# Optimization experiments

Measured on AMD Instinct MI355X. Metric: run time of the kernel, lower is better.

The kernel has to match this reference:

```python
import jax, jax.numpy as jnp
import numpy as np

D = 768  # in_channels == out_channels (forced by residual + shared LayerNorm)
B, S = 8, 2048


def setup_inputs() -> dict:
    key = jax.random.key(0)
    ks = jax.random.split(key, 5)
    x = jax.random.normal(ks[0], (B, S, D), dtype=jnp.float32)
    # LayerNorm params
    ln_g = jnp.ones((D,), dtype=jnp.float32)
    ln_b = jnp.zeros((D,), dtype=jnp.float32)
    # Q/K linear params (torch Linear: y = x @ W.T + b)
    scale = 1.0 / np.sqrt(D)
    Wq = jax.random.uniform(ks[1], (D, D), jnp.float32, -scale, scale)
    bq = jax.random.uniform(ks[2], (D,), jnp.float32, -scale, scale)
    Wk = jax.random.uniform(ks[3], (D, D), jnp.float32, -scale, scale)
    bk = jax.random.uniform(ks[4], (D,), jnp.float32, -scale, scale)
    return {"x": x, "ln_g": ln_g, "ln_b": ln_b, "Wq": Wq, "bq": bq, "Wk": Wk, "bk": bk}


def _layernorm(x, g, b, eps=1e-5):
    mu = jnp.mean(x, axis=-1, keepdims=True)
    var = jnp.mean(jnp.square(x - mu), axis=-1, keepdims=True)
    return (x - mu) * jax.lax.rsqrt(var + eps) * g + b


def reference(x, ln_g, ln_b, Wq, bq, Wk, bk):
    origin = x
    xn = _layernorm(x, ln_g, ln_b)
    Q = xn @ Wq.T + bq  # [B,S,D]
    K = xn @ Wk.T + bk  # [B,S,D]
    scores = jnp.einsum('bsd,btd->bst', Q, K) / jnp.sqrt(jnp.asarray(D, x.dtype))
    attn = jax.nn.softmax(scores, axis=-1)  # [B,S,S]
    out = jnp.einsum('bst,btd->bsd', attn, origin) + origin
    # note: original then computes relu(layernorm(out)) but returns `out` (dead code)
    return out
```

## Files before the change

### kernel.cpp

```cpp
#include <hip/hip_runtime.h>

typedef __bf16 bf16;
typedef __bf16 v8bf __attribute__((ext_vector_type(8)));
typedef __bf16 v4bf __attribute__((ext_vector_type(4)));
typedef float  v4f  __attribute__((ext_vector_type(4)));

__device__ __forceinline__ void gload_lds16(const void* g, void* l) {
    __builtin_amdgcn_global_load_lds(
        (const __attribute__((address_space(1))) void*)g,
        (__attribute__((address_space(3))) void*)l, 16, 0, 0);
}

__global__ __launch_bounds__(256)
void ln_cast(const float* __restrict__ x, const float* __restrict__ g,
             const float* __restrict__ b, bf16* __restrict__ xn,
             bf16* __restrict__ xv)
{
    const long row = blockIdx.x;
    const float* xr = x + row * 768;
    const int tid = threadIdx.x;
    const int wave = tid >> 6, lane = tid & 63;

    float a0 = xr[tid], a1 = xr[tid + 256], a2 = xr[tid + 512];
    float s = a0 + a1 + a2;
    #pragma unroll
    for (int off = 32; off; off >>= 1) s += __shfl_xor(s, off);
    __shared__ float sh[4], sh2[4];
    if (!lane) sh[wave] = s;
    __syncthreads();
    const float mu = (sh[0] + sh[1] + sh[2] + sh[3]) * (1.0f / 768.0f);

    float d0 = a0 - mu, d1 = a1 - mu, d2 = a2 - mu;
    float ss = d0 * d0 + d1 * d1 + d2 * d2;
    #pragma unroll
    for (int off = 32; off; off >>= 1) ss += __shfl_xor(ss, off);
    if (!lane) sh2[wave] = ss;
    __syncthreads();
    const float var = (sh2[0] + sh2[1] + sh2[2] + sh2[3]) * (1.0f / 768.0f);
    const float rstd = rsqrtf(var + 1e-5f);

    bf16* xnr = xn + row * 768;
    bf16* xvr = xv + row * 768;
    xnr[tid]       = (bf16)(d0 * rstd * g[tid]       + b[tid]);
    xnr[tid + 256] = (bf16)(d1 * rstd * g[tid + 256] + b[tid + 256]);
    xnr[tid + 512] = (bf16)(d2 * rstd * g[tid + 512] + b[tid + 512]);
    xvr[tid]       = (bf16)a0;
    xvr[tid + 256] = (bf16)a1;
    xvr[tid + 512] = (bf16)a2;
}

__global__ __launch_bounds__(256)
void cvt_w(const float* __restrict__ Wq, const float* __restrict__ Wk,
           bf16* __restrict__ Wcat)
{
    const int z = blockIdx.y;
    const float* src = z ? Wk : Wq;
    bf16* dst = Wcat + (long)z * 768 * 768;
    const int i = (blockIdx.x * 256 + threadIdx.x) * 4;
    const float4 v = *(const float4*)(src + i);
    v4bf o = {(bf16)v.x, (bf16)v.y, (bf16)v.z, (bf16)v.w};
    *(v4bf*)(dst + i) = o;
}

__global__ __launch_bounds__(256)
void transpose_bf(const bf16* __restrict__ in, bf16* __restrict__ outT)
{
    __shared__ __attribute__((aligned(16))) bf16 tile[64 * 64];
    const int t0 = blockIdx.x * 64, d0 = blockIdx.y * 64;
    in   += (long)blockIdx.z * 2048 * 768;
    outT += (long)blockIdx.z * 768 * 2048;
    const int tid = threadIdx.x;

    #pragma unroll
    for (int it = 0; it < 2; ++it) {
        const int lin = it * 256 + tid;
        const int r = lin >> 3;
        const int g = lin & 7;
        const int pg = g ^ (r & 7) ^ ((r >> 3) & 7);
        v8bf v = *(const v8bf*)(in + (long)(t0 + r) * 768 + d0 + g * 8);
        *(v8bf*)(tile + r * 64 + pg * 8) = v;
    }
    __syncthreads();
    #pragma unroll
    for (int it = 0; it < 2; ++it) {
        const int lin = it * 256 + tid;
        const int dd = lin >> 3;
        const int tb = lin & 7;
        v8bf o;
        #pragma unroll
        for (int j = 0; j < 8; ++j) {
            const int t = tb * 8 + j;
            const int pg = (dd >> 3) ^ (t & 7) ^ ((t >> 3) & 7);
            o[j] = tile[t * 64 + pg * 8 + (dd & 7)];
        }
        *(v8bf*)(outT + (long)(d0 + dd) * 2048 + t0 + tb * 8) = o;
    }
}

__global__ __launch_bounds__(256)
void gemm_qk(const bf16* __restrict__ A, const bf16* __restrict__ W,
             const float* __restrict__ bq, const float* __restrict__ bk,
             float qscale, bf16* __restrict__ Qb, bf16* __restrict__ Kb)
{
    __shared__ __attribute__((aligned(16))) bf16 As[2][128 * 32];
    __shared__ __attribute__((aligned(16))) bf16 Bs[2][128 * 32];

    const int bx = blockIdx.x;
    const int r = bx & 7, j = bx >> 3;
    const int m0 = (r * 16 + j / 12) * 128;
    const int n0 = (j % 12) * 128;

    const int tid = threadIdx.x, wave = tid >> 6, lane = tid & 63;
    const bf16* Ab = A + (long)m0 * 768;
    const bf16* Bb = W + (long)n0 * 768;

    const int lrow = lane >> 2;
    const int lk   = (lane & 3) * 8;
    const int wm = (wave >> 1) * 64, wn = (wave & 1) * 64;
    const int lr = lane & 15, lq = lane >> 4;

    v4f acc[4][4] = {};

    for (int kk = 0; kk < 768; kk += 64) {
        #pragma unroll
        for (int p = 0; p < 2; ++p)
            #pragma unroll
            for (int it = 0; it < 2; ++it) {
                const int c = it * 4 + wave;
                const int row = c * 16 + lrow;
                gload_lds16(Ab + (long)row * 768 + kk + p * 32 + lk,
                            (char*)As[p] + c * 1024);
                gload_lds16(Bb + (long)row * 768 + kk + p * 32 + lk,
                            (char*)Bs[p] + c * 1024);
            }
        __syncthreads();

        #pragma unroll
        for (int p = 0; p < 2; ++p) {
            v8bf af[4], bfr[4];
            #pragma unroll
            for (int i = 0; i < 4; ++i)
                af[i] = *(const v8bf*)(As[p] + (wm + i * 16 + lr) * 32 + lq * 8);
            #pragma unroll
            for (int jj = 0; jj < 4; ++jj)
                bfr[jj] = *(const v8bf*)(Bs[p] + (wn + jj * 16 + lr) * 32 + lq * 8);
            #pragma unroll
            for (int i = 0; i < 4; ++i)
                #pragma unroll
                for (int jj = 0; jj < 4; ++jj)
                    acc[i][jj] = __builtin_amdgcn_mfma_f32_16x16x32_bf16(
                        af[i], bfr[jj], acc[i][jj], 0, 0, 0);
        }
        __syncthreads();
    }

    const bool isQ = (n0 < 768);
    const float* bias = isQ ? bq : bk;
    const float sc = isQ ? qscale : 1.0f;
    bf16* C = isQ ? Qb : Kb;
    const int c0 = isQ ? n0 : n0 - 768;

    #pragma unroll
    for (int i = 0; i < 4; ++i) {
        #pragma unroll
        for (int rr = 0; rr < 4; ++rr) {
            const int row = m0 + wm + i * 16 + lq * 4 + rr;
            #pragma unroll
            for (int jj = 0; jj < 4; ++jj) {
                const int col = c0 + wn + jj * 16 + lr;
                C[(long)row * 768 + col] = (bf16)((acc[i][jj][rr] + bias[col]) * sc);
            }
        }
    }
}

__global__ __launch_bounds__(256)
void gemm_scores(const bf16* __restrict__ Q, const bf16* __restrict__ K,
                 bf16* __restrict__ S)
{
    __shared__ __attribute__((aligned(16))) bf16 As[2][128 * 32];
    __shared__ __attribute__((aligned(16))) bf16 Bs[2][128 * 32];

    const int bx = blockIdx.x;
    const int batch = bx & 7, j = bx >> 3;
    const int m0 = (j >> 4) * 128, n0 = (j & 15) * 128;

    const bf16* Ab = Q + (long)batch * 2048 * 768 + (long)m0 * 768;
    const bf16* Bb = K + (long)batch * 2048 * 768 + (long)n0 * 768;
    bf16* C = S + (long)batch * 2048 * 2048;

    const int tid = threadIdx.x, wave = tid >> 6, lane = tid & 63;
    const int lrow = lane >> 2;
    const int lk   = (lane & 3) * 8;
    const int wm = (wave >> 1) * 64, wn = (wave & 1) * 64;
    const int lr = lane & 15, lq = lane >> 4;

    v4f acc[4][4] = {};

    for (int kk = 0; kk < 768; kk += 64) {
        #pragma unroll
        for (int p = 0; p < 2; ++p)
            #pragma unroll
            for (int it = 0; it < 2; ++it) {
                const int c = it * 4 + wave;
                const int row = c * 16 + lrow;
                gload_lds16(Ab + (long)row * 768 + kk + p * 32 + lk,
                            (char*)As[p] + c * 1024);
                gload_lds16(Bb + (long)row * 768 + kk + p * 32 + lk,
                            (char*)Bs[p] + c * 1024);
            }
        __syncthreads();

        #pragma unroll
        for (int p = 0; p < 2; ++p) {
            v8bf af[4], bfr[4];
            #pragma unroll
            for (int i = 0; i < 4; ++i)
                af[i] = *(const v8bf*)(As[p] + (wm + i * 16 + lr) * 32 + lq * 8);
            #pragma unroll
            for (int jj = 0; jj < 4; ++jj)
                bfr[jj] = *(const v8bf*)(Bs[p] + (wn + jj * 16 + lr) * 32 + lq * 8);
            #pragma unroll
            for (int i = 0; i < 4; ++i)
                #pragma unroll
                for (int jj = 0; jj < 4; ++jj)
                    acc[i][jj] = __builtin_amdgcn_mfma_f32_16x16x32_bf16(
                        af[i], bfr[jj], acc[i][jj], 0, 0, 0);
        }
        __syncthreads();
    }

    #pragma unroll
    for (int i = 0; i < 4; ++i) {
        #pragma unroll
        for (int rr = 0; rr < 4; ++rr) {
            const int row = m0 + wm + i * 16 + lq * 4 + rr;
            #pragma unroll
            for (int jj = 0; jj < 4; ++jj) {
                const int col = n0 + wn + jj * 16 + lr;
                C[(long)row * 2048 + col] = (bf16)acc[i][jj][rr];
            }
        }
    }
}

__global__ __launch_bounds__(256)
void softmax_rows(bf16* __restrict__ S)
{
    const long row = blockIdx.x;
    bf16* p = S + row * 2048 + threadIdx.x * 8;
    const int wave = threadIdx.x >> 6, lane = threadIdx.x & 63;

    v8bf raw = *(const v8bf*)p;
    float v[8];
    float mx = -1e30f;
    #pragma unroll
    for (int j = 0; j < 8; ++j) { v[j] = (float)raw[j]; mx = fmaxf(mx, v[j]); }
    #pragma unroll
    for (int off = 32; off; off >>= 1) mx = fmaxf(mx, __shfl_xor(mx, off));
    __shared__ float shm[4], shs[4];
    if (!lane) shm[wave] = mx;
    __syncthreads();
    mx = fmaxf(fmaxf(shm[0], shm[1]), fmaxf(shm[2], shm[3]));

    float s = 0.f;
    #pragma unroll
    for (int j = 0; j < 8; ++j) { v[j] = __expf(v[j] - mx); s += v[j]; }
    #pragma unroll
    for (int off = 32; off; off >>= 1) s += __shfl_xor(s, off);
    if (!lane) shs[wave] = s;
    __syncthreads();
    const float inv = 1.0f / (shs[0] + shs[1] + shs[2] + shs[3]);

    v8bf o;
    #pragma unroll
    for (int j = 0; j < 8; ++j) o[j] = (bf16)(v[j] * inv);
    *(v8bf*)p = o;
}

__global__ __launch_bounds__(256)
void gemm_pv(const bf16* __restrict__ P, const bf16* __restrict__ VT,
             const float* __restrict__ Xres, float* __restrict__ Out)
{
    __shared__ __attribute__((aligned(16))) bf16 As[2][64 * 32];
    __shared__ __attribute__((aligned(16))) bf16 Bs[2][128 * 32];

    const int bx = blockIdx.x;
    const int batch = bx & 7, j = bx >> 3;
    const int m0 = (j / 6) * 64;
    const int n0 = (j % 6) * 128;

    const bf16* Ab = P  + (long)batch * 2048 * 2048 + (long)m0 * 2048;
    const bf16* Bb = VT + (long)batch * 768 * 2048  + (long)n0 * 2048;
    const float* Xr = Xres + (long)batch * 2048 * 768;
    float* O = Out + (long)batch * 2048 * 768;

    const int tid = threadIdx.x, wave = tid >> 6, lane = tid & 63;
    const int lrow = lane >> 2;
    const int lk   = (lane & 3) * 8;
    const int wm = (wave >> 1) * 32, wn = (wave & 1) * 64;
    const int lr = lane & 15, lq = lane >> 4;

    v4f acc[2][4] = {};

    for (int kk = 0; kk < 2048; kk += 64) {
        #pragma unroll
        for (int p = 0; p < 2; ++p) {
            gload_lds16(Ab + (long)(wave * 16 + lrow) * 2048 + kk + p * 32 + lk,
                        (char*)As[p] + wave * 1024);
            #pragma unroll
            for (int it = 0; it < 2; ++it) {
                const int c = it * 4 + wave;
                gload_lds16(Bb + (long)(c * 16 + lrow) * 2048 + kk + p * 32 + lk,
                            (char*)Bs[p] + c * 1024);
            }
        }
        __syncthreads();

        #pragma unroll
        for (int p = 0; p < 2; ++p) {
            v8bf af[2], bfr[4];
            #pragma unroll
            for (int i = 0; i < 2; ++i)
                af[i] = *(const v8bf*)(As[p] + (wm + i * 16 + lr) * 32 + lq * 8);
            #pragma unroll
            for (int jj = 0; jj < 4; ++jj)
                bfr[jj] = *(const v8bf*)(Bs[p] + (wn + jj * 16 + lr) * 32 + lq * 8);
            #pragma unroll
            for (int i = 0; i < 2; ++i)
                #pragma unroll
                for (int jj = 0; jj < 4; ++jj)
                    acc[i][jj] = __builtin_amdgcn_mfma_f32_16x16x32_bf16(
                        af[i], bfr[jj], acc[i][jj], 0, 0, 0);
        }
        __syncthreads();
    }

    #pragma unroll
    for (int i = 0; i < 2; ++i) {
        #pragma unroll
        for (int rr = 0; rr < 4; ++rr) {
            const int row = m0 + wm + i * 16 + lq * 4 + rr;
            #pragma unroll
            for (int jj = 0; jj < 4; ++jj) {
                const int col = n0 + wn + jj * 16 + lr;
                const long idx = (long)row * 768 + col;
                O[idx] = acc[i][jj][rr] + Xr[idx];
            }
        }
    }
}

extern "C" void kernel_launch(void* const* d_in, const int* in_sizes, int n_in,
                              void* d_out, int out_size, void* d_ws, size_t ws_size,
                              hipStream_t stream)
{
    const float* x    = (const float*)d_in[0];
    const float* ln_g = (const float*)d_in[1];
    const float* ln_b = (const float*)d_in[2];
    const float* Wq   = (const float*)d_in[3];
    const float* bq   = (const float*)d_in[4];
    const float* Wk   = (const float*)d_in[5];
    const float* bk   = (const float*)d_in[6];
    float* out = (float*)d_out;

    const long R = 8L * 2048;
    char* ws = (char*)d_ws;
    size_t off = 0;
    auto take = [&](size_t bytes) -> char* {
        char* p = ws + off;
        off += (bytes + 255) & ~(size_t)255;
        return p;
    };
    bf16* xn   = (bf16*)take(R * 768 * 2);
    bf16* xv   = (bf16*)take(R * 768 * 2);
    bf16* Qb   = (bf16*)take(R * 768 * 2);
    bf16* Kb   = (bf16*)take(R * 768 * 2);
    bf16* Wcat = (bf16*)take(1536L * 768 * 2);
    bf16* Sc   = (bf16*)take(8L * 2048 * 2048 * 2);

    ln_cast<<<R, 256, 0, stream>>>(x, ln_g, ln_b, xn, xv);
    cvt_w<<<dim3(576, 2), 256, 0, stream>>>(Wq, Wk, Wcat);

    const float qscale = 0.036084391824351615f;
    gemm_qk<<<1536, 256, 0, stream>>>(xn, Wcat, bq, bk, qscale, Qb, Kb);

    bf16* xvT = xn;
    transpose_bf<<<dim3(32, 12, 8), 256, 0, stream>>>(xv, xvT);

    gemm_scores<<<2048, 256, 0, stream>>>(Qb, Kb, Sc);
    softmax_rows<<<16384, 256, 0, stream>>>(Sc);
    gemm_pv<<<1536, 256, 0, stream>>>(Sc, xvT, x, out);
}
```

Before: 340.9 us.

## Fuse softmax exp into scores GEMM and defer normalization to PV epilogue

Removes the standalone softmax kernel. The scores GEMM epilogue now writes exp(score) directly and accumulates per-row sums with atomics into a buffer that ln_cast zeroes, and the PV GEMM divides by that row sum in its epilogue. The score tiles are also remapped into 4x4 groups to improve L2 reuse of Q and K. This saves a full read and write of the 8x2048x2048 bf16 score matrix and one launch. In exchange it drops max-subtraction, so exp can overflow if scores grow large, and the atomic row sums make the accumulation order nondeterministic.

```diff
diff --git a/kernel.cpp b/kernel.cpp
--- a/kernel.cpp
+++ b/kernel.cpp
@@ -14,12 +14,14 @@
 __global__ __launch_bounds__(256)
 void ln_cast(const float* __restrict__ x, const float* __restrict__ g,
              const float* __restrict__ b, bf16* __restrict__ xn,
-             bf16* __restrict__ xv)
+             bf16* __restrict__ xv, float* __restrict__ L)
 {
     const long row = blockIdx.x;
     const float* xr = x + row * 768;
     const int tid = threadIdx.x;
     const int wave = tid >> 6, lane = tid & 63;
+
+    if (row < 64) L[row * 256 + tid] = 0.0f;
 
     float a0 = xr[tid], a1 = xr[tid + 256], a2 = xr[tid + 512];
     float s = a0 + a1 + a2;
@@ -176,18 +178,22 @@
 
 __global__ __launch_bounds__(256)
 void gemm_scores(const bf16* __restrict__ Q, const bf16* __restrict__ K,
-                 bf16* __restrict__ S)
+                 bf16* __restrict__ E, float* __restrict__ L)
 {
     __shared__ __attribute__((aligned(16))) bf16 As[2][128 * 32];
     __shared__ __attribute__((aligned(16))) bf16 Bs[2][128 * 32];
 
     const int bx = blockIdx.x;
     const int batch = bx & 7, j = bx >> 3;
-    const int m0 = (j >> 4) * 128, n0 = (j & 15) * 128;
+    const int st = j >> 4, w = j & 15;
+    const int mt = (st >> 2) * 4 + (w >> 2);
+    const int nt = (st & 3) * 4 + (w & 3);
+    const int m0 = mt * 128, n0 = nt * 128;
 
     const bf16* Ab = Q + (long)batch * 2048 * 768 + (long)m0 * 768;
     const bf16* Bb = K + (long)batch * 2048 * 768 + (long)n0 * 768;
-    bf16* C = S + (long)batch * 2048 * 2048;
+    bf16* C = E + (long)batch * 2048 * 2048;
+    float* Lb = L + (long)batch * 2048;
 
     const int tid = threadIdx.x, wave = tid >> 6, lane = tid & 63;
     const int lrow = lane >> 2;
@@ -235,52 +241,28 @@
         #pragma unroll
         for (int rr = 0; rr < 4; ++rr) {
             const int row = m0 + wm + i * 16 + lq * 4 + rr;
+            float e[4], rs = 0.f;
+            #pragma unroll
+            for (int jj = 0; jj < 4; ++jj) {
+                e[jj] = __expf(acc[i][jj][rr]);
+                rs += e[jj];
+            }
+            #pragma unroll
+            for (int off = 1; off < 16; off <<= 1) rs += __shfl_xor(rs, off);
+            if (lr == 0) atomicAdd(&Lb[row], rs);
             #pragma unroll
             for (int jj = 0; jj < 4; ++jj) {
                 const int col = n0 + wn + jj * 16 + lr;
-                C[(long)row * 2048 + col] = (bf16)acc[i][jj][rr];
-            }
-        }
-    }
-}
-
-__global__ __launch_bounds__(256)
-void softmax_rows(bf16* __restrict__ S)
-{
-    const long row = blockIdx.x;
-    bf16* p = S + row * 2048 + threadIdx.x * 8;
-    const int wave = threadIdx.x >> 6, lane = threadIdx.x & 63;
-
-    v8bf raw = *(const v8bf*)p;
-    float v[8];
-    float mx = -1e30f;
-    #pragma unroll
-    for (int j = 0; j < 8; ++j) { v[j] = (float)raw[j]; mx = fmaxf(mx, v[j]); }
-    #pragma unroll
-    for (int off = 32; off; off >>= 1) mx = fmaxf(mx, __shfl_xor(mx, off));
-    __shared__ float shm[4], shs[4];
-    if (!lane) shm[wave] = mx;
-    __syncthreads();
-    mx = fmaxf(fmaxf(shm[0], shm[1]), fmaxf(shm[2], shm[3]));
-
-    float s = 0.f;
-    #pragma unroll
-    for (int j = 0; j < 8; ++j) { v[j] = __expf(v[j] - mx); s += v[j]; }
-    #pragma unroll
-    for (int off = 32; off; off >>= 1) s += __shfl_xor(s, off);
-    if (!lane) shs[wave] = s;
-    __syncthreads();
-    const float inv = 1.0f / (shs[0] + shs[1] + shs[2] + shs[3]);
-
-    v8bf o;
-    #pragma unroll
-    for (int j = 0; j < 8; ++j) o[j] = (bf16)(v[j] * inv);
-    *(v8bf*)p = o;
+                C[(long)row * 2048 + col] = (bf16)e[jj];
+            }
+        }
+    }
 }
 
 __global__ __launch_bounds__(256)
 void gemm_pv(const bf16* __restrict__ P, const bf16* __restrict__ VT,
-             const float* __restrict__ Xres, float* __restrict__ Out)
+             const float* __restrict__ L, const float* __restrict__ Xres,
+             float* __restrict__ Out)
 {
     __shared__ __attribute__((aligned(16))) bf16 As[2][64 * 32];
     __shared__ __attribute__((aligned(16))) bf16 Bs[2][128 * 32];
@@ -292,6 +274,7 @@
 
     const bf16* Ab = P  + (long)batch * 2048 * 2048 + (long)m0 * 2048;
     const bf16* Bb = VT + (long)batch * 768 * 2048  + (long)n0 * 2048;
+    const float* Lb = L + (long)batch * 2048;
     const float* Xr = Xres + (long)batch * 2048 * 768;
     float* O = Out + (long)batch * 2048 * 768;
 
@@ -341,11 +324,12 @@
         #pragma unroll
         for (int rr = 0; rr < 4; ++rr) {
             const int row = m0 + wm + i * 16 + lq * 4 + rr;
+            const float invL = 1.0f / Lb[row];
             #pragma unroll
             for (int jj = 0; jj < 4; ++jj) {
                 const int col = n0 + wn + jj * 16 + lr;
                 const long idx = (long)row * 768 + col;
-                O[idx] = acc[i][jj][rr] + Xr[idx];
+                O[idx] = acc[i][jj][rr] * invL + Xr[idx];
             }
         }
     }
@@ -372,14 +356,15 @@
         off += (bytes + 255) & ~(size_t)255;
         return p;
     };
-    bf16* xn   = (bf16*)take(R * 768 * 2);
-    bf16* xv   = (bf16*)take(R * 768 * 2);
-    bf16* Qb   = (bf16*)take(R * 768 * 2);
-    bf16* Kb   = (bf16*)take(R * 768 * 2);
-    bf16* Wcat = (bf16*)take(1536L * 768 * 2);
-    bf16* Sc   = (bf16*)take(8L * 2048 * 2048 * 2);
-
-    ln_cast<<<R, 256, 0, stream>>>(x, ln_g, ln_b, xn, xv);
+    bf16*  xn   = (bf16*)take(R * 768 * 2);
+    bf16*  xv   = (bf16*)take(R * 768 * 2);
+    bf16*  Qb   = (bf16*)take(R * 768 * 2);
+    bf16*  Kb   = (bf16*)take(R * 768 * 2);
+    bf16*  Wcat = (bf16*)take(1536L * 768 * 2);
+    float* Lrow = (float*)take(R * 4);
+    bf16*  Sc   = (bf16*)take(8L * 2048 * 2048 * 2);
+
+    ln_cast<<<R, 256, 0, stream>>>(x, ln_g, ln_b, xn, xv, Lrow);
     cvt_w<<<dim3(576, 2), 256, 0, stream>>>(Wq, Wk, Wcat);
 
     const float qscale = 0.036084391824351615f;
@@ -388,7 +373,6 @@
     bf16* xvT = xn;
     transpose_bf<<<dim3(32, 12, 8), 256, 0, stream>>>(xv, xvT);
 
-    gemm_scores<<<2048, 256, 0, stream>>>(Qb, Kb, Sc);
-    softmax_rows<<<16384, 256, 0, stream>>>(Sc);
-    gemm_pv<<<1536, 256, 0, stream>>>(Sc, xvT, x, out);
-}
+    gemm_scores<<<2048, 256, 0, stream>>>(Qb, Kb, Sc, Lrow);
+    gemm_pv<<<1536, 256, 0, stream>>>(Sc, xvT, Lrow, x, out);
+}
```

New measurement: 329.2 us. 1.04x faster.
